# Kernel tuning notes

Hardware: AMD Instinct MI355X
Metric: run time of the kernel (lower is better)

Reference implementation:

```python
import jax, jax.numpy as jnp
import numpy as np

N = 50000      # nodes
E = 1600000    # edges (avg degree 32)
F_IN = 256     # input feature dim
H = 128        # hidden == output size of GCN
C = 40         # num_class


def setup_inputs() -> dict:
    key = jax.random.key(0)
    ks = jax.random.split(key, 13)
    inp = {
        "features": jax.random.normal(ks[0], (N, F_IN), dtype=jnp.float32),
        "src": jax.random.randint(ks[1], (E,), 0, N, dtype=jnp.int32),
        "dst": jax.random.randint(ks[2], (E,), 0, N, dtype=jnp.int32),
        "edge_weight": jax.random.uniform(ks[3], (E,), dtype=jnp.float32),
        "y": jax.random.normal(ks[4], (N, C), dtype=jnp.float32),
        # GCN layer 1
        "W1": jax.random.normal(ks[5], (F_IN, H), dtype=jnp.float32) / np.sqrt(F_IN),
        "b1": jnp.zeros((H,), dtype=jnp.float32),
        # GCN layer 2
        "W2": jax.random.normal(ks[6], (H, H), dtype=jnp.float32) / np.sqrt(H),
        "b2": jnp.zeros((H,), dtype=jnp.float32),
        # y_fc_emb: Linear(num_class, output_size)
        "We": jax.random.normal(ks[7], (C, H), dtype=jnp.float32) / np.sqrt(C),
        "be": jnp.zeros((H,), dtype=jnp.float32),
        # y_fc: Linear(hidden*2, num_class)
        "Wf": jax.random.normal(ks[8], (2 * H, C), dtype=jnp.float32) / np.sqrt(2 * H),
        "bf": jnp.zeros((C,), dtype=jnp.float32),
    }
    return inp


def _spmm(edge_weight, src, dst, x, n):
    # (sparse adj) @ x : out[i] = sum_{(j->i)} w_ji * x[j]
    return jax.ops.segment_sum(edge_weight[:, None] * x[src], dst, num_segments=n)


def reference(features, src, dst, edge_weight, y, W1, b1, W2, b2, We, be, Wf, bf):
    n = features.shape[0]
    # F.normalize: L2 row-normalize with eps=1e-12 clamp
    norm = jnp.maximum(jnp.linalg.norm(features, axis=1, keepdims=True), 1e-12)
    x = features / norm
    # GCN layer 1: relu(adj @ (x @ W1) + b1)   (dropout = 0)
    h = jax.nn.relu(_spmm(edge_weight, src, dst, x @ W1, n) + b1)
    # GCN layer 2: adj @ (h @ W2) + b2
    h = _spmm(edge_weight, src, dst, h @ W2, n) + b2
    # label embedding + head
    y_emb = y @ We + be
    logits = jnp.concatenate([y_emb, h], axis=1) @ Wf + bf
    return jax.nn.softmax(logits, axis=-1)
```

## Files before the change

kernel.cpp:

```cpp
#include <hip/hip_runtime.h>
#include <hip/hip_bf16.h>
#include <hip/hip_fp16.h>
#include <cstdint>
#include <cstddef>
#include <cmath>

#define F_IN 256
#define HDIM 128
#define CCLS 40
#define NBMAX 1024
#define EPB 4096
#define CAP 4096

typedef short bf16x8 __attribute__((ext_vector_type(8)));
typedef float f32x4 __attribute__((ext_vector_type(4)));

__device__ inline unsigned pkbf(float a, float b) {
  __hip_bfloat162 h = __float22bfloat162_rn(make_float2(a, b));
  unsigned u;
  __builtin_memcpy(&u, &h, 4);
  return u;
}
__device__ inline unsigned short bfr(float f) {
  __hip_bfloat16 h = __float2bfloat16(f);
  unsigned short u;
  __builtin_memcpy(&u, &h, 2);
  return u;
}
__device__ inline float f16tof(unsigned short hb) {
  __half hv;
  __builtin_memcpy(&hv, &hb, 2);
  return __half2float(hv);
}
__device__ inline unsigned short ftof16(float f) {
  __half hv = __float2half(f);
  unsigned short u;
  __builtin_memcpy(&u, &hv, 2);
  return u;
}

__device__ inline void gemm1_body(char* smem, int bm0, const float* __restrict__ X,
                                  const unsigned short* __restrict__ WT,
                                  unsigned short* __restrict__ C, int M, int t) {
  unsigned short (*As)[264] = (unsigned short(*)[264])smem;
  const int w8 = t >> 6, l = t & 63;

  for (int rr = 0; rr < 16; ++rr) {
    int row = w8 * 16 + rr;
    int grow = bm0 + row;
    const float* p = X + (size_t)(grow < M ? grow : (M - 1)) * F_IN + l * 4;
    float4 v = *(const float4*)p;
    float s = v.x * v.x + v.y * v.y + v.z * v.z + v.w * v.w;
#pragma unroll
    for (int off = 32; off; off >>= 1) s += __shfl_xor(s, off, 64);
    float inv = 1.0f / fmaxf(sqrtf(s), 1e-12f);
    *(uint2*)&As[row][l * 4] =
        make_uint2(pkbf(v.x * inv, v.y * inv), pkbf(v.z * inv, v.w * inv));
  }

  const int ln = l & 15, quad = l >> 4;
  const int m0 = bm0 + w8 * 16;
  f32x4 acc[8];
#pragma unroll
  for (int i = 0; i < 8; ++i) acc[i] = (f32x4){0.f, 0.f, 0.f, 0.f};

#pragma unroll
  for (int k0 = 0; k0 < F_IN; k0 += 32) {
    bf16x8 af = *(const bf16x8*)&As[w8 * 16 + ln][k0 + quad * 8];
#pragma unroll
    for (int ti = 0; ti < 8; ++ti) {
      bf16x8 bfv = *(const bf16x8*)(WT + (size_t)(ti * 16 + ln) * F_IN + k0 + quad * 8);
      acc[ti] = __builtin_amdgcn_mfma_f32_16x16x32_bf16(af, bfv, acc[ti], 0, 0, 0);
    }
  }

#pragma unroll
  for (int r = 0; r < 4; ++r) {
    int grow = m0 + quad * 4 + r;
    if (grow < M) {
      unsigned short* cp = C + (size_t)grow * HDIM + ln;
#pragma unroll
      for (int ti = 0; ti < 8; ++ti) cp[ti * 16] = bfr(acc[ti][r]);
    }
  }
}

__global__ __launch_bounds__(256) void prep_kernel(const float* __restrict__ W1,
                                                   unsigned short* __restrict__ W1T,
                                                   int* __restrict__ gcursor, int nb) {
  const int b = blockIdx.x;
  const int t = threadIdx.x;
  if (b < 128) {
    int idx = b * 256 + t;
    int nr = idx >> 8, k = idx & 255;
    W1T[idx] = bfr(W1[k * 128 + nr]);
  } else {
    for (int i = t; i < nb; i += 256) gcursor[i] = 0;
  }
}

__global__ __launch_bounds__(256) void scatter_gemm1(const int* __restrict__ src,
                                                     const int* __restrict__ dst,
                                                     const float* __restrict__ w,
                                                     int* __restrict__ gcursor,
                                                     uint2* __restrict__ ews,
                                                     const float* __restrict__ X,
                                                     const unsigned short* __restrict__ W1T,
                                                     unsigned short* __restrict__ C,
                                                     const float* __restrict__ W2,
                                                     unsigned short* __restrict__ W2T,
                                                     const float* __restrict__ We,
                                                     const float* __restrict__ be,
                                                     const float* __restrict__ Wf,
                                                     const float* __restrict__ bf,
                                                     float* __restrict__ Wc,
                                                     float* __restrict__ bc,
                                                     int e, int nb, int nsb, int ngb,
                                                     int M) {
  __shared__ char smem[64 * 264 * 2];
  const int t = threadIdx.x;
  const int b = blockIdx.x;
  if (b < nsb) {
    int* hist = (int*)smem;
    int* sb   = hist + NBMAX;
    for (int i = t; i < nb; i += 256) hist[i] = 0;
    __syncthreads();
    const int b4 = b * (EPB / 4);
    int4 dv[4];
    int rk[16];
#pragma unroll
    for (int k = 0; k < 4; ++k) {
      int gi = b4 + k * 256 + t;
      int e0 = gi * 4;
      int4 d = make_int4(-1, -1, -1, -1);
      if (e0 + 3 < e) d = ((const int4*)dst)[gi];
      else if (e0 < e) {
        d.x = dst[e0];
        if (e0 + 1 < e) d.y = dst[e0 + 1];
        if (e0 + 2 < e) d.z = dst[e0 + 2];
      }
      dv[k] = d;
      rk[k * 4 + 0] = (d.x >= 0) ? atomicAdd(&hist[d.x >> 6], 1) : 0;
      rk[k * 4 + 1] = (d.y >= 0) ? atomicAdd(&hist[d.y >> 6], 1) : 0;
      rk[k * 4 + 2] = (d.z >= 0) ? atomicAdd(&hist[d.z >> 6], 1) : 0;
      rk[k * 4 + 3] = (d.w >= 0) ? atomicAdd(&hist[d.w >> 6], 1) : 0;
    }
    __syncthreads();
    for (int i = t; i < nb; i += 256) {
      int c = hist[i];
      sb[i] = i * CAP + (c ? atomicAdd(&gcursor[i], c) : 0);
    }
    __syncthreads();
#pragma unroll
    for (int k = 0; k < 4; ++k) {
      int gi = b4 + k * 256 + t;
      int e0 = gi * 4;
      if (e0 >= e) continue;
      int4 s4 = make_int4(0, 0, 0, 0);
      float4 w4 = make_float4(0.f, 0.f, 0.f, 0.f);
      if (e0 + 3 < e) { s4 = ((const int4*)src)[gi]; w4 = ((const float4*)w)[gi]; }
      else {
        s4.x = src[e0]; w4.x = w[e0];
        if (e0 + 1 < e) { s4.y = src[e0 + 1]; w4.y = w[e0 + 1]; }
        if (e0 + 2 < e) { s4.z = src[e0 + 2]; w4.z = w[e0 + 2]; }
      }
      int4 d = dv[k];
      if (d.x >= 0) ews[sb[d.x >> 6] + rk[k * 4 + 0]] =
          make_uint2(((unsigned)(d.x & 63) << 26) | (unsigned)s4.x, __float_as_uint(w4.x));
      if (d.y >= 0) ews[sb[d.y >> 6] + rk[k * 4 + 1]] =
          make_uint2(((unsigned)(d.y & 63) << 26) | (unsigned)s4.y, __float_as_uint(w4.y));
      if (d.z >= 0) ews[sb[d.z >> 6] + rk[k * 4 + 2]] =
          make_uint2(((unsigned)(d.z & 63) << 26) | (unsigned)s4.z, __float_as_uint(w4.z));
      if (d.w >= 0) ews[sb[d.w >> 6] + rk[k * 4 + 3]] =
          make_uint2(((unsigned)(d.w & 63) << 26) | (unsigned)s4.w, __float_as_uint(w4.w));
    }
  } else if (b < nsb + ngb) {
    gemm1_body(smem, (b - nsb) * 64, X, W1T, C, M, t);
  } else if (b < nsb + ngb + 64) {
    int idx = (b - nsb - ngb) * 256 + t;
    int nr = idx >> 7, k = idx & 127;
    W2T[idx] = bfr(W2[k * 128 + nr]);
  } else {
    int part = b - (nsb + ngb + 64);
    int lo = part * 800, hi = lo + 800;
    for (int i = lo + t; i < hi; i += 256) {
      int c = i / CCLS, j = i % CCLS;
      float s = 0.f;
      for (int f = 0; f < HDIM; ++f) s += We[c * HDIM + f] * Wf[f * CCLS + j];
      Wc[i] = s;
    }
    if (part == 0 && t < CCLS) {
      float s = bf[t];
      for (int f = 0; f < HDIM; ++f) s += be[f] * Wf[f * CCLS + t];
      bc[t] = s;
    }
  }
}

__global__ __launch_bounds__(256) void bucket_sort(const uint2* __restrict__ ews,
                                                   const int* __restrict__ gcursor,
                                                   unsigned* __restrict__ ews2,
                                                   int* __restrict__ row_off,
                                                   int* __restrict__ row_end,
                                                   int n, int nb) {
  __shared__ int cnt[256];
  __shared__ int cur[64];
  const int t = threadIdx.x;
  const int b = blockIdx.x;
  cnt[t] = 0;
  __syncthreads();
  const int base = b * CAP;
  const int c = gcursor[b];
  const int wv = t >> 6;
  for (int i = t; i < c; i += 256)
    atomicAdd(&cnt[wv * 64 + ((unsigned)ews[base + i].x >> 26)], 1);
  __syncthreads();
  if (t < 64) {
    int tot = cnt[t] + cnt[64 + t] + cnt[128 + t] + cnt[192 + t];
    int x = tot;
#pragma unroll
    for (int off = 1; off < 64; off <<= 1) {
      int y = __shfl_up(x, off, 64);
      if (t >= off) x += y;
    }
    int excl = x - tot;
    cur[t] = excl;
    int node = b * 64 + t;
    if (node < n) { row_off[node] = base + excl; row_end[node] = base + excl + tot; }
  }
  __syncthreads();
  for (int i = t; i < c; i += 256) {
    uint2 p = ews[base + i];
    int d = (unsigned)p.x >> 26;
    int pos = base + atomicAdd(&cur[d], 1);
    ews2[pos] = (p.x & 0xFFFFu) | ((unsigned)ftof16(__uint_as_float(p.y)) << 16);
  }
}

#define SPMM_PAIR(ua, ub)                                                      \
  {                                                                            \
    unsigned u = half ? (ub) : (ua);                                           \
    float wt = f16tof((unsigned short)(u >> 16));                              \
    const uint2 xv = *(const uint2*)(xin + (size_t)(u & 0xFFFFu) * HDIM + fo); \
    acc.x = fmaf(wt, __uint_as_float(xv.x << 16), acc.x);                      \
    acc.y = fmaf(wt, __uint_as_float(xv.x & 0xFFFF0000u), acc.y);              \
    acc.z = fmaf(wt, __uint_as_float(xv.y << 16), acc.z);                      \
    acc.w = fmaf(wt, __uint_as_float(xv.y & 0xFFFF0000u), acc.w);              \
  }

template <int OUT_BF16>
__global__ __launch_bounds__(256) void spmm_bf16(const unsigned short* __restrict__ xin,
                                                 const unsigned* __restrict__ ews,
                                                 const int* __restrict__ row_off,
                                                 const int* __restrict__ row_end,
                                                 const float* __restrict__ bias,
                                                 void* __restrict__ outp, int n,
                                                 int do_relu) {
  const int t = threadIdx.x;
  const int l = t & 63;
  const int node = blockIdx.x * 4 + (t >> 6);
  if (node >= n) return;
  const int ue0 = __builtin_amdgcn_readfirstlane(row_off[node]);
  const int ue1 = __builtin_amdgcn_readfirstlane(row_end[node]);
  const int cnt = ue1 - ue0;
  const unsigned* ep = ews + ue0;
  const int fo = (l & 31) * 4;
  const int half = l >> 5;
  float4 acc = make_float4(0.f, 0.f, 0.f, 0.f);

  int k = 0;
  for (; k + 16 <= cnt; k += 16) {
    unsigned a0 = ep[k + 0], a1 = ep[k + 1], a2 = ep[k + 2], a3 = ep[k + 3];
    unsigned a4 = ep[k + 4], a5 = ep[k + 5], a6 = ep[k + 6], a7 = ep[k + 7];
    unsigned a8 = ep[k + 8], a9 = ep[k + 9], a10 = ep[k + 10], a11 = ep[k + 11];
    unsigned a12 = ep[k + 12], a13 = ep[k + 13], a14 = ep[k + 14], a15 = ep[k + 15];
    SPMM_PAIR(a0, a1);
    SPMM_PAIR(a2, a3);
    SPMM_PAIR(a4, a5);
    SPMM_PAIR(a6, a7);
    SPMM_PAIR(a8, a9);
    SPMM_PAIR(a10, a11);
    SPMM_PAIR(a12, a13);
    SPMM_PAIR(a14, a15);
  }
  for (; k + 8 <= cnt; k += 8) {
    unsigned a0 = ep[k + 0], a1 = ep[k + 1], a2 = ep[k + 2], a3 = ep[k + 3];
    unsigned a4 = ep[k + 4], a5 = ep[k + 5], a6 = ep[k + 6], a7 = ep[k + 7];
    SPMM_PAIR(a0, a1);
    SPMM_PAIR(a2, a3);
    SPMM_PAIR(a4, a5);
    SPMM_PAIR(a6, a7);
  }
  for (; k < cnt; k += 2) {
    unsigned a0 = ep[k];
    unsigned a1 = (k + 1 < cnt) ? ep[k + 1] : 0u;
    SPMM_PAIR(a0, a1);
  }

  acc.x += __shfl_xor(acc.x, 32, 64);
  acc.y += __shfl_xor(acc.y, 32, 64);
  acc.z += __shfl_xor(acc.z, 32, 64);
  acc.w += __shfl_xor(acc.w, 32, 64);
  if (l < 32) {
    float4 bv = *(const float4*)(bias + fo);
    float4 r = make_float4(acc.x + bv.x, acc.y + bv.y, acc.z + bv.z, acc.w + bv.w);
    if (do_relu) {
      r.x = fmaxf(r.x, 0.f); r.y = fmaxf(r.y, 0.f);
      r.z = fmaxf(r.z, 0.f); r.w = fmaxf(r.w, 0.f);
    }
    if (OUT_BF16) {
      uint2 o = make_uint2(pkbf(r.x, r.y), pkbf(r.z, r.w));
      *(uint2*)((unsigned short*)outp + (size_t)node * HDIM + fo) = o;
    } else {
      *(float4*)((float*)outp + (size_t)node * HDIM + fo) = r;
    }
  }
}

template <int K>
__global__ __launch_bounds__(256) void gemm_mfma(const unsigned short* __restrict__ A,
                                                 const unsigned short* __restrict__ WT,
                                                 unsigned short* __restrict__ C, int M) {
  const int t = threadIdx.x;
  const int w = t >> 6, l = t & 63;
  const int ln = l & 15, quad = l >> 4;
  const int m0 = blockIdx.x * 64 + w * 16;
  const int arow = m0 + ln;
  const unsigned short* aptr = A + (size_t)(arow < M ? arow : (M - 1)) * K + quad * 8;

  f32x4 acc[8];
#pragma unroll
  for (int i = 0; i < 8; ++i) acc[i] = (f32x4){0.f, 0.f, 0.f, 0.f};

#pragma unroll
  for (int k0 = 0; k0 < K; k0 += 32) {
    bf16x8 af = *(const bf16x8*)(aptr + k0);
#pragma unroll
    for (int ti = 0; ti < 8; ++ti) {
      bf16x8 bfv = *(const bf16x8*)(WT + (size_t)(ti * 16 + ln) * K + k0 + quad * 8);
      acc[ti] = __builtin_amdgcn_mfma_f32_16x16x32_bf16(af, bfv, acc[ti], 0, 0, 0);
    }
  }

#pragma unroll
  for (int r = 0; r < 4; ++r) {
    int grow = m0 + quad * 4 + r;
    if (grow < M) {
      unsigned short* cp = C + (size_t)grow * HDIM + ln;
#pragma unroll
      for (int ti = 0; ti < 8; ++ti) cp[ti * 16] = bfr(acc[ti][r]);
    }
  }
}

__global__ __launch_bounds__(256) void head_kernel(const float* __restrict__ y,
                                                   const float* __restrict__ h2,
                                                   const float* __restrict__ Wc,
                                                   const float* __restrict__ bc,
                                                   const float* __restrict__ Wf,
                                                   float* __restrict__ out, int n) {
  __shared__ float sW[169 * CCLS];
  const int t = threadIdx.x;
  for (int i = t; i < 400; i += 256) ((float4*)sW)[i] = ((const float4*)Wc)[i];
  for (int i = t; i < 1280; i += 256)
    ((float4*)(sW + CCLS * CCLS))[i] = ((const float4*)(Wf + HDIM * CCLS))[i];
  if (t < 10) ((float4*)(sW + 168 * CCLS))[t] = ((const float4*)bc)[t];
  __syncthreads();

  const int node = blockIdx.x * 256 + t;
  const int nc = node < n ? node : n - 1;
  const float* zy = y + (size_t)nc * CCLS;
  const float* zh = h2 + (size_t)nc * HDIM;

  float acc[40];
#pragma unroll
  for (int cq = 0; cq < 10; ++cq) {
    float4 b4 = *(const float4*)&sW[168 * CCLS + cq * 4];
    acc[cq * 4 + 0] = b4.x; acc[cq * 4 + 1] = b4.y;
    acc[cq * 4 + 2] = b4.z; acc[cq * 4 + 3] = b4.w;
  }

#pragma unroll 2
  for (int kc = 0; kc < 10; ++kc) {
    float4 zv = *(const float4*)(zy + kc * 4);
    float zj[4] = {zv.x, zv.y, zv.z, zv.w};
#pragma unroll
    for (int j = 0; j < 4; ++j) {
      const float* wr = sW + (kc * 4 + j) * CCLS;
#pragma unroll
      for (int cq = 0; cq < 10; ++cq) {
        float4 w4 = *(const float4*)(wr + cq * 4);
        acc[cq * 4 + 0] = fmaf(zj[j], w4.x, acc[cq * 4 + 0]);
        acc[cq * 4 + 1] = fmaf(zj[j], w4.y, acc[cq * 4 + 1]);
        acc[cq * 4 + 2] = fmaf(zj[j], w4.z, acc[cq * 4 + 2]);
        acc[cq * 4 + 3] = fmaf(zj[j], w4.w, acc[cq * 4 + 3]);
      }
    }
  }
#pragma unroll 2
  for (int kc = 0; kc < 32; ++kc) {
    float4 zv = *(const float4*)(zh + kc * 4);
    float zj[4] = {zv.x, zv.y, zv.z, zv.w};
#pragma unroll
    for (int j = 0; j < 4; ++j) {
      const float* wr = sW + (40 + kc * 4 + j) * CCLS;
#pragma unroll
      for (int cq = 0; cq < 10; ++cq) {
        float4 w4 = *(const float4*)(wr + cq * 4);
        acc[cq * 4 + 0] = fmaf(zj[j], w4.x, acc[cq * 4 + 0]);
        acc[cq * 4 + 1] = fmaf(zj[j], w4.y, acc[cq * 4 + 1]);
        acc[cq * 4 + 2] = fmaf(zj[j], w4.z, acc[cq * 4 + 2]);
        acc[cq * 4 + 3] = fmaf(zj[j], w4.w, acc[cq * 4 + 3]);
      }
    }
  }

  float m = acc[0];
#pragma unroll
  for (int c = 1; c < 40; ++c) m = fmaxf(m, acc[c]);
  float sum = 0.f;
#pragma unroll
  for (int c = 0; c < 40; ++c) { acc[c] = __expf(acc[c] - m); sum += acc[c]; }
  float inv = 1.0f / sum;
  if (node < n) {
    float* op = out + (size_t)node * CCLS;
#pragma unroll
    for (int cq = 0; cq < 10; ++cq) {
      float4 o = make_float4(acc[cq * 4 + 0] * inv, acc[cq * 4 + 1] * inv,
                             acc[cq * 4 + 2] * inv, acc[cq * 4 + 3] * inv);
      *(float4*)(op + cq * 4) = o;
    }
  }
}

extern "C" void kernel_launch(void* const* d_in, const int* in_sizes, int n_in,
                              void* d_out, int out_size, void* d_ws, size_t ws_size,
                              hipStream_t stream) {
  (void)n_in; (void)out_size; (void)ws_size;
  const float* features = (const float*)d_in[0];
  const int*   src      = (const int*)d_in[1];
  const int*   dst      = (const int*)d_in[2];
  const float* ew       = (const float*)d_in[3];
  const float* y        = (const float*)d_in[4];
  const float* W1       = (const float*)d_in[5];
  const float* b1       = (const float*)d_in[6];
  const float* W2       = (const float*)d_in[7];
  const float* b2       = (const float*)d_in[8];
  const float* We       = (const float*)d_in[9];
  const float* be       = (const float*)d_in[10];
  const float* Wf       = (const float*)d_in[11];
  const float* bf       = (const float*)d_in[12];
  float* out = (float*)d_out;

  const int n = in_sizes[0] / F_IN;
  const int e = in_sizes[1];
  const int nb = (n + 63) >> 6;

  char* w = (char*)d_ws;
  auto take = [&](size_t bytes) {
    char* p = w;
    w += (bytes + 255) & ~(size_t)255;
    return p;
  };
  int*   gcursor  = (int*)take((size_t)nb * 4);
  int*   row_off  = (int*)take((size_t)n * 4);
  int*   row_end  = (int*)take((size_t)n * 4);
  uint2* ews      = (uint2*)take((size_t)nb * CAP * 8);
  unsigned* ews2  = (unsigned*)take((size_t)nb * CAP * 4);
  unsigned short* bufH1  = (unsigned short*)take((size_t)n * HDIM * 2);
  unsigned short* bufH2  = (unsigned short*)take((size_t)n * HDIM * 2);
  float* bufS     = (float*)take((size_t)n * HDIM * 4);
  unsigned short* W1T = (unsigned short*)take((size_t)HDIM * F_IN * 2);
  unsigned short* W2T = (unsigned short*)take((size_t)HDIM * HDIM * 2);
  float* Wc       = (float*)take(CCLS * CCLS * 4);
  float* bc       = (float*)take(CCLS * 4);

  const int nsb = (e + EPB - 1) / EPB;
  const int ngb = (n + 63) / 64;

  prep_kernel<<<129, 256, 0, stream>>>(W1, W1T, gcursor, nb);
  scatter_gemm1<<<nsb + ngb + 64 + 2, 256, 0, stream>>>(
      src, dst, ew, gcursor, ews, features, W1T, bufH1,
      W2, W2T, We, be, Wf, bf, Wc, bc, e, nb, nsb, ngb, n);
  bucket_sort<<<nb, 256, 0, stream>>>(ews, gcursor, ews2, row_off, row_end, n, nb);

  spmm_bf16<1><<<(n + 3) / 4, 256, 0, stream>>>(bufH1, ews2, row_off, row_end, b1,
                                                bufH2, n, 1);
  gemm_mfma<HDIM><<<(n + 63) / 64, 256, 0, stream>>>(bufH2, W2T, bufH1, n);
  spmm_bf16<0><<<(n + 3) / 4, 256, 0, stream>>>(bufH1, ews2, row_off, row_end, b2,
                                                bufS, n, 0);
  head_kernel<<<(n + 255) / 256, 256, 0, stream>>>(y, bufS, Wc, bc, Wf, out, n);
}
```

Baseline: 343.9 us.

## Fuse layer-1 SpMM with W2 GEMM and retile GEMM1 to 16-row blocks

Merges the first SpMM (with bias and ReLU) and the following W2 GEMM into one kernel. Each block aggregates 16 nodes into shared memory and then runs MFMA on them, so the intermediate bf16 H round trip and one launch go away. GEMM1 in the scatter kernel is retiled to 16 rows per block, with each wave covering 32 output columns, which means more blocks and less shared memory each. Scatter blocks now take 8192 edges each. Smaller GEMM tiles re-read W1T/W2T more often, and bigger scatter blocks cut parallelism in the histogram phase.

```diff
diff --git a/kernel.cpp b/kernel.cpp
--- a/kernel.cpp
+++ b/kernel.cpp
@@ -9,7 +9,7 @@
 #define HDIM 128
 #define CCLS 40
 #define NBMAX 1024
-#define EPB 4096
+#define EPB 8192
 #define CAP 4096
 
 typedef short bf16x8 __attribute__((ext_vector_type(8)));
@@ -37,52 +37,6 @@
   unsigned short u;
   __builtin_memcpy(&u, &hv, 2);
   return u;
-}
-
-__device__ inline void gemm1_body(char* smem, int bm0, const float* __restrict__ X,
-                                  const unsigned short* __restrict__ WT,
-                                  unsigned short* __restrict__ C, int M, int t) {
-  unsigned short (*As)[264] = (unsigned short(*)[264])smem;
-  const int w8 = t >> 6, l = t & 63;
-
-  for (int rr = 0; rr < 16; ++rr) {
-    int row = w8 * 16 + rr;
-    int grow = bm0 + row;
-    const float* p = X + (size_t)(grow < M ? grow : (M - 1)) * F_IN + l * 4;
-    float4 v = *(const float4*)p;
-    float s = v.x * v.x + v.y * v.y + v.z * v.z + v.w * v.w;
-#pragma unroll
-    for (int off = 32; off; off >>= 1) s += __shfl_xor(s, off, 64);
-    float inv = 1.0f / fmaxf(sqrtf(s), 1e-12f);
-    *(uint2*)&As[row][l * 4] =
-        make_uint2(pkbf(v.x * inv, v.y * inv), pkbf(v.z * inv, v.w * inv));
-  }
-
-  const int ln = l & 15, quad = l >> 4;
-  const int m0 = bm0 + w8 * 16;
-  f32x4 acc[8];
-#pragma unroll
-  for (int i = 0; i < 8; ++i) acc[i] = (f32x4){0.f, 0.f, 0.f, 0.f};
-
-#pragma unroll
-  for (int k0 = 0; k0 < F_IN; k0 += 32) {
-    bf16x8 af = *(const bf16x8*)&As[w8 * 16 + ln][k0 + quad * 8];
-#pragma unroll
-    for (int ti = 0; ti < 8; ++ti) {
-      bf16x8 bfv = *(const bf16x8*)(WT + (size_t)(ti * 16 + ln) * F_IN + k0 + quad * 8);
-      acc[ti] = __builtin_amdgcn_mfma_f32_16x16x32_bf16(af, bfv, acc[ti], 0, 0, 0);
-    }
-  }
-
-#pragma unroll
-  for (int r = 0; r < 4; ++r) {
-    int grow = m0 + quad * 4 + r;
-    if (grow < M) {
-      unsigned short* cp = C + (size_t)grow * HDIM + ln;
-#pragma unroll
-      for (int ti = 0; ti < 8; ++ti) cp[ti * 16] = bfr(acc[ti][r]);
-    }
-  }
 }
 
 __global__ __launch_bounds__(256) void prep_kernel(const float* __restrict__ W1,
@@ -117,7 +71,7 @@
                                                      float* __restrict__ bc,
                                                      int e, int nb, int nsb, int ngb,
                                                      int M) {
-  __shared__ char smem[64 * 264 * 2];
+  __shared__ char smem[16 * 264 * 2];
   const int t = threadIdx.x;
   const int b = blockIdx.x;
   if (b < nsb) {
@@ -126,10 +80,10 @@
     for (int i = t; i < nb; i += 256) hist[i] = 0;
     __syncthreads();
     const int b4 = b * (EPB / 4);
-    int4 dv[4];
-    int rk[16];
-#pragma unroll
-    for (int k = 0; k < 4; ++k) {
+    int4 dv[8];
+    int rk[32];
+#pragma unroll
+    for (int k = 0; k < 8; ++k) {
       int gi = b4 + k * 256 + t;
       int e0 = gi * 4;
       int4 d = make_int4(-1, -1, -1, -1);
@@ -152,7 +106,7 @@
     }
     __syncthreads();
 #pragma unroll
-    for (int k = 0; k < 4; ++k) {
+    for (int k = 0; k < 8; ++k) {
       int gi = b4 + k * 256 + t;
       int e0 = gi * 4;
       if (e0 >= e) continue;
@@ -175,7 +129,45 @@
           make_uint2(((unsigned)(d.w & 63) << 26) | (unsigned)s4.w, __float_as_uint(w4.w));
     }
   } else if (b < nsb + ngb) {
-    gemm1_body(smem, (b - nsb) * 64, X, W1T, C, M, t);
+    unsigned short (*As)[264] = (unsigned short(*)[264])smem;
+    const int w8 = t >> 6, l = t & 63;
+    const int bm0 = (b - nsb) * 16;
+    for (int rr = 0; rr < 4; ++rr) {
+      int row = w8 * 4 + rr;
+      int grow = bm0 + row;
+      const float* p = X + (size_t)(grow < M ? grow : (M - 1)) * F_IN + l * 4;
+      float4 v = *(const float4*)p;
+      float s = v.x * v.x + v.y * v.y + v.z * v.z + v.w * v.w;
+#pragma unroll
+      for (int off = 32; off; off >>= 1) s += __shfl_xor(s, off, 64);
+      float inv = 1.0f / fmaxf(sqrtf(s), 1e-12f);
+      *(uint2*)&As[row][l * 4] =
+          make_uint2(pkbf(v.x * inv, v.y * inv), pkbf(v.z * inv, v.w * inv));
+    }
+    __syncthreads();
+    const int ln = l & 15, quad = l >> 4;
+    f32x4 acc[2];
+    acc[0] = (f32x4){0.f, 0.f, 0.f, 0.f};
+    acc[1] = (f32x4){0.f, 0.f, 0.f, 0.f};
+#pragma unroll
+    for (int k0 = 0; k0 < F_IN; k0 += 32) {
+      bf16x8 af = *(const bf16x8*)&As[ln][k0 + quad * 8];
+#pragma unroll
+      for (int ti = 0; ti < 2; ++ti) {
+        bf16x8 bfv = *(const bf16x8*)(W1T + (size_t)(w8 * 32 + ti * 16 + ln) * F_IN +
+                                      k0 + quad * 8);
+        acc[ti] = __builtin_amdgcn_mfma_f32_16x16x32_bf16(af, bfv, acc[ti], 0, 0, 0);
+      }
+    }
+#pragma unroll
+    for (int r = 0; r < 4; ++r) {
+      int grow = bm0 + quad * 4 + r;
+      if (grow < M) {
+#pragma unroll
+        for (int ti = 0; ti < 2; ++ti)
+          C[(size_t)grow * HDIM + w8 * 32 + ti * 16 + ln] = bfr(acc[ti][r]);
+      }
+    }
   } else if (b < nsb + ngb + 64) {
     int idx = (b - nsb - ngb) * 256 + t;
     int nr = idx >> 7, k = idx & 127;
@@ -248,14 +240,98 @@
     acc.w = fmaf(wt, __uint_as_float(xv.y & 0xFFFF0000u), acc.w);              \
   }
 
-template <int OUT_BF16>
-__global__ __launch_bounds__(256) void spmm_bf16(const unsigned short* __restrict__ xin,
-                                                 const unsigned* __restrict__ ews,
-                                                 const int* __restrict__ row_off,
-                                                 const int* __restrict__ row_end,
-                                                 const float* __restrict__ bias,
-                                                 void* __restrict__ outp, int n,
-                                                 int do_relu) {
+#define SPMM_NODE_LOOP(ep, cnt)                                                 \
+  int k = 0;                                                                    \
+  for (; k + 16 <= cnt; k += 16) {                                              \
+    unsigned a0 = ep[k + 0], a1 = ep[k + 1], a2 = ep[k + 2], a3 = ep[k + 3];    \
+    unsigned a4 = ep[k + 4], a5 = ep[k + 5], a6 = ep[k + 6], a7 = ep[k + 7];    \
+    unsigned a8 = ep[k + 8], a9 = ep[k + 9], a10 = ep[k + 10], a11 = ep[k + 11];\
+    unsigned a12 = ep[k + 12], a13 = ep[k + 13], a14 = ep[k + 14],              \
+             a15 = ep[k + 15];                                                  \
+    SPMM_PAIR(a0, a1); SPMM_PAIR(a2, a3); SPMM_PAIR(a4, a5); SPMM_PAIR(a6, a7); \
+    SPMM_PAIR(a8, a9); SPMM_PAIR(a10, a11); SPMM_PAIR(a12, a13);                \
+    SPMM_PAIR(a14, a15);                                                        \
+  }                                                                             \
+  for (; k + 8 <= cnt; k += 8) {                                                \
+    unsigned a0 = ep[k + 0], a1 = ep[k + 1], a2 = ep[k + 2], a3 = ep[k + 3];    \
+    unsigned a4 = ep[k + 4], a5 = ep[k + 5], a6 = ep[k + 6], a7 = ep[k + 7];    \
+    SPMM_PAIR(a0, a1); SPMM_PAIR(a2, a3); SPMM_PAIR(a4, a5); SPMM_PAIR(a6, a7); \
+  }                                                                             \
+  for (; k < cnt; k += 2) {                                                     \
+    unsigned a0 = ep[k];                                                        \
+    unsigned a1 = (k + 1 < cnt) ? ep[k + 1] : 0u;                               \
+    SPMM_PAIR(a0, a1);                                                          \
+  }
+
+__global__ __launch_bounds__(256) void spmm1_gemm2(const unsigned short* __restrict__ xin,
+                                                   const unsigned* __restrict__ ews,
+                                                   const int* __restrict__ row_off,
+                                                   const int* __restrict__ row_end,
+                                                   const float* __restrict__ bias,
+                                                   const unsigned short* __restrict__ W2T,
+                                                   unsigned short* __restrict__ C,
+                                                   int n) {
+  __shared__ unsigned short As[16][136];
+  const int t = threadIdx.x;
+  const int l = t & 63;
+  const int w = t >> 6;
+  const int fo = (l & 31) * 4;
+  const int half = l >> 5;
+  const int nb0 = blockIdx.x * 16;
+#pragma unroll
+  for (int j = 0; j < 4; ++j) {
+    const int node = nb0 + w * 4 + j;
+    if (node < n) {
+      const int ue0 = __builtin_amdgcn_readfirstlane(row_off[node]);
+      const int ue1 = __builtin_amdgcn_readfirstlane(row_end[node]);
+      const int cnt = ue1 - ue0;
+      const unsigned* ep = ews + ue0;
+      float4 acc = make_float4(0.f, 0.f, 0.f, 0.f);
+      SPMM_NODE_LOOP(ep, cnt)
+      acc.x += __shfl_xor(acc.x, 32, 64);
+      acc.y += __shfl_xor(acc.y, 32, 64);
+      acc.z += __shfl_xor(acc.z, 32, 64);
+      acc.w += __shfl_xor(acc.w, 32, 64);
+      if (l < 32) {
+        float4 bv = *(const float4*)(bias + fo);
+        float r0 = fmaxf(acc.x + bv.x, 0.f), r1 = fmaxf(acc.y + bv.y, 0.f);
+        float r2 = fmaxf(acc.z + bv.z, 0.f), r3 = fmaxf(acc.w + bv.w, 0.f);
+        *(uint2*)&As[w * 4 + j][fo] = make_uint2(pkbf(r0, r1), pkbf(r2, r3));
+      }
+    }
+  }
+  __syncthreads();
+  const int ln = l & 15, quad = l >> 4;
+  f32x4 acc2[2];
+  acc2[0] = (f32x4){0.f, 0.f, 0.f, 0.f};
+  acc2[1] = (f32x4){0.f, 0.f, 0.f, 0.f};
+#pragma unroll
+  for (int k0 = 0; k0 < HDIM; k0 += 32) {
+    bf16x8 af = *(const bf16x8*)&As[ln][k0 + quad * 8];
+#pragma unroll
+    for (int ti = 0; ti < 2; ++ti) {
+      bf16x8 bfv = *(const bf16x8*)(W2T + (size_t)(w * 32 + ti * 16 + ln) * HDIM +
+                                    k0 + quad * 8);
+      acc2[ti] = __builtin_amdgcn_mfma_f32_16x16x32_bf16(af, bfv, acc2[ti], 0, 0, 0);
+    }
+  }
+#pragma unroll
+  for (int r = 0; r < 4; ++r) {
+    int grow = nb0 + quad * 4 + r;
+    if (grow < n) {
+#pragma unroll
+      for (int ti = 0; ti < 2; ++ti)
+        C[(size_t)grow * HDIM + w * 32 + ti * 16 + ln] = bfr(acc2[ti][r]);
+    }
+  }
+}
+
+__global__ __launch_bounds__(256) void spmm_f32(const unsigned short* __restrict__ xin,
+                                                const unsigned* __restrict__ ews,
+                                                const int* __restrict__ row_off,
+                                                const int* __restrict__ row_end,
+                                                const float* __restrict__ bias,
+                                                float* __restrict__ outp, int n) {
   const int t = threadIdx.x;
   const int l = t & 63;
   const int node = blockIdx.x * 4 + (t >> 6);
@@ -267,89 +343,15 @@
   const int fo = (l & 31) * 4;
   const int half = l >> 5;
   float4 acc = make_float4(0.f, 0.f, 0.f, 0.f);
-
-  int k = 0;
-  for (; k + 16 <= cnt; k += 16) {
-    unsigned a0 = ep[k + 0], a1 = ep[k + 1], a2 = ep[k + 2], a3 = ep[k + 3];
-    unsigned a4 = ep[k + 4], a5 = ep[k + 5], a6 = ep[k + 6], a7 = ep[k + 7];
-    unsigned a8 = ep[k + 8], a9 = ep[k + 9], a10 = ep[k + 10], a11 = ep[k + 11];
-    unsigned a12 = ep[k + 12], a13 = ep[k + 13], a14 = ep[k + 14], a15 = ep[k + 15];
-    SPMM_PAIR(a0, a1);
-    SPMM_PAIR(a2, a3);
-    SPMM_PAIR(a4, a5);
-    SPMM_PAIR(a6, a7);
-    SPMM_PAIR(a8, a9);
-    SPMM_PAIR(a10, a11);
-    SPMM_PAIR(a12, a13);
-    SPMM_PAIR(a14, a15);
-  }
-  for (; k + 8 <= cnt; k += 8) {
-    unsigned a0 = ep[k + 0], a1 = ep[k + 1], a2 = ep[k + 2], a3 = ep[k + 3];
-    unsigned a4 = ep[k + 4], a5 = ep[k + 5], a6 = ep[k + 6], a7 = ep[k + 7];
-    SPMM_PAIR(a0, a1);
-    SPMM_PAIR(a2, a3);
-    SPMM_PAIR(a4, a5);
-    SPMM_PAIR(a6, a7);
-  }
-  for (; k < cnt; k += 2) {
-    unsigned a0 = ep[k];
-    unsigned a1 = (k + 1 < cnt) ? ep[k + 1] : 0u;
-    SPMM_PAIR(a0, a1);
-  }
-
+  SPMM_NODE_LOOP(ep, cnt)
   acc.x += __shfl_xor(acc.x, 32, 64);
   acc.y += __shfl_xor(acc.y, 32, 64);
   acc.z += __shfl_xor(acc.z, 32, 64);
   acc.w += __shfl_xor(acc.w, 32, 64);
   if (l < 32) {
     float4 bv = *(const float4*)(bias + fo);
-    float4 r = make_float4(acc.x + bv.x, acc.y + bv.y, acc.z + bv.z, acc.w + bv.w);
-    if (do_relu) {
-      r.x = fmaxf(r.x, 0.f); r.y = fmaxf(r.y, 0.f);
-      r.z = fmaxf(r.z, 0.f); r.w = fmaxf(r.w, 0.f);
-    }
-    if (OUT_BF16) {
-      uint2 o = make_uint2(pkbf(r.x, r.y), pkbf(r.z, r.w));
-      *(uint2*)((unsigned short*)outp + (size_t)node * HDIM + fo) = o;
-    } else {
-      *(float4*)((float*)outp + (size_t)node * HDIM + fo) = r;
-    }
-  }
-}
-
-template <int K>
-__global__ __launch_bounds__(256) void gemm_mfma(const unsigned short* __restrict__ A,
-                                                 const unsigned short* __restrict__ WT,
-                                                 unsigned short* __restrict__ C, int M) {
-  const int t = threadIdx.x;
-  const int w = t >> 6, l = t & 63;
-  const int ln = l & 15, quad = l >> 4;
-  const int m0 = blockIdx.x * 64 + w * 16;
-  const int arow = m0 + ln;
-  const unsigned short* aptr = A + (size_t)(arow < M ? arow : (M - 1)) * K + quad * 8;
-
-  f32x4 acc[8];
-#pragma unroll
-  for (int i = 0; i < 8; ++i) acc[i] = (f32x4){0.f, 0.f, 0.f, 0.f};
-
-#pragma unroll
-  for (int k0 = 0; k0 < K; k0 += 32) {
-    bf16x8 af = *(const bf16x8*)(aptr + k0);
-#pragma unroll
-    for (int ti = 0; ti < 8; ++ti) {
-      bf16x8 bfv = *(const bf16x8*)(WT + (size_t)(ti * 16 + ln) * K + k0 + quad * 8);
-      acc[ti] = __builtin_amdgcn_mfma_f32_16x16x32_bf16(af, bfv, acc[ti], 0, 0, 0);
-    }
-  }
-
-#pragma unroll
-  for (int r = 0; r < 4; ++r) {
-    int grow = m0 + quad * 4 + r;
-    if (grow < M) {
-      unsigned short* cp = C + (size_t)grow * HDIM + ln;
-#pragma unroll
-      for (int ti = 0; ti < 8; ++ti) cp[ti * 16] = bfr(acc[ti][r]);
-    }
+    *(float4*)(outp + (size_t)node * HDIM + fo) =
+        make_float4(acc.x + bv.x, acc.y + bv.y, acc.z + bv.z, acc.w + bv.w);
   }
 }
 
@@ -476,7 +478,7 @@
   float* bc       = (float*)take(CCLS * 4);
 
   const int nsb = (e + EPB - 1) / EPB;
-  const int ngb = (n + 63) / 64;
+  const int ngb = (n + 15) / 16;
 
   prep_kernel<<<129, 256, 0, stream>>>(W1, W1T, gcursor, nb);
   scatter_gemm1<<<nsb + ngb + 64 + 2, 256, 0, stream>>>(
@@ -484,10 +486,8 @@
       W2, W2T, We, be, Wf, bf, Wc, bc, e, nb, nsb, ngb, n);
   bucket_sort<<<nb, 256, 0, stream>>>(ews, gcursor, ews2, row_off, row_end, n, nb);
 
-  spmm_bf16<1><<<(n + 3) / 4, 256, 0, stream>>>(bufH1, ews2, row_off, row_end, b1,
-                                                bufH2, n, 1);
-  gemm_mfma<HDIM><<<(n + 63) / 64, 256, 0, stream>>>(bufH2, W2T, bufH1, n);
-  spmm_bf16<0><<<(n + 3) / 4, 256, 0, stream>>>(bufH1, ews2, row_off, row_end, b2,
-                                                bufS, n, 0);
+  spmm1_gemm2<<<(n + 15) / 16, 256, 0, stream>>>(bufH1, ews2, row_off, row_end, b1,
+                                                 W2T, bufH2, n);
+  spmm_f32<<<(n + 3) / 4, 256, 0, stream>>>(bufH2, ews2, row_off, row_end, b2, bufS, n);
   head_kernel<<<(n + 255) / 256, 256, 0, stream>>>(y, bufS, Wc, bc, Wf, out, n);
 }
```

Result: faster. 325.3 us (-5.4%).
